# Optimization experiments

Measured on AMD Instinct MI355X. Metric: run time of the kernel, lower is better.

## Reference

```python
import jax, jax.numpy as jnp
import numpy as np

K = 64  # num_struct_elements


def rational_hat(pts, mask, centers, radius):
    """pts: (B,P,D), mask: (B,P), centers: (K,D), radius: scalar -> (B,K).

    f(x,c) = 1/(1+||x-c||_1) - 1/(1+| |r| - ||x-c||_1 |), masked sum over points.
    """
    # L1 distance to every center: (B,P,K)
    d = jnp.sum(jnp.abs(pts[:, :, None, :] - centers[None, None, :, :]), axis=-1)
    f = 1.0 / (1.0 + d) - 1.0 / (1.0 + jnp.abs(jnp.abs(radius) - d))
    # mask dummy points and reduce over the point axis -> (B,K)
    return jnp.einsum('bpk,bp->bk', f, mask)


def setup_inputs() -> dict:
    key = jax.random.key(0)
    ks = jax.random.split(key, 6)
    B, P0, PE = 128, 4096, 1024
    inp = {
        'h_0': jax.random.normal(ks[0], (B, P0, 2), dtype=jnp.float32),
        'mask_0': jnp.ones((B, P0), dtype=jnp.float32),
        'h_0_ess': jax.random.normal(ks[1], (B, PE, 1), dtype=jnp.float32),
        'mask_0_ess': jnp.ones((B, PE), dtype=jnp.float32),
        'h_1_ess': jax.random.normal(ks[2], (B, PE, 1), dtype=jnp.float32),
        'mask_1_ess': jnp.ones((B, PE), dtype=jnp.float32),
        # learned parameters: centers ~ N(0,1) (torchph default init), radius init 0.1
        'centers_0': jax.random.normal(ks[3], (K, 2), dtype=jnp.float32),
        'radius_0': jnp.float32(0.1),
        'centers_0_ess': jax.random.normal(ks[4], (K, 1), dtype=jnp.float32),
        'radius_0_ess': jnp.float32(0.1),
        'centers_1_ess': jax.random.normal(ks[5], (K, 1), dtype=jnp.float32),
        'radius_1_ess': jnp.float32(0.1),
    }
    return inp


def reference(h_0, mask_0, h_0_ess, mask_0_ess, h_1_ess, mask_1_ess,
              centers_0, radius_0, centers_0_ess, radius_0_ess,
              centers_1_ess, radius_1_ess):
    x0 = rational_hat(h_0, mask_0, centers_0, radius_0)
    x0e = rational_hat(h_0_ess, mask_0_ess, centers_0_ess, radius_0_ess)
    x1e = rational_hat(h_1_ess, mask_1_ess, centers_1_ess, radius_1_ess)
    return jnp.concatenate([x0, x0e, x1e], axis=1)  # (B, 3K)
```

## Files before the change

kernel.cpp:

```cpp
#include <hip/hip_runtime.h>

#define TPB 256
#define NW  (TPB / 64)
#define PPB 1024
#define PPW (PPB / NW)
#define PAIRS_PER_WAVE (PPW / 2)

typedef float v2f __attribute__((ext_vector_type(2)));

static __device__ __forceinline__ v2f vabs2(v2f v) {
    return __builtin_elementwise_max(v, -v);
}

__global__ __launch_bounds__(TPB) void pershom_kernel(
    const float* __restrict__ h0,  const float* __restrict__ m0,
    const float* __restrict__ h0e, const float* __restrict__ m0e,
    const float* __restrict__ h1e, const float* __restrict__ m1e,
    const float* __restrict__ c0,  const float* __restrict__ r0,
    const float* __restrict__ c0e, const float* __restrict__ r0e,
    const float* __restrict__ c1e, const float* __restrict__ r1e,
    float* __restrict__ out)
{
    __shared__ float4 pxy[PPB / 2];
    __shared__ v2f    pm [PPB / 2];
    __shared__ float  partial[NW][64];

    const int bid = blockIdx.x;
    const int tid = threadIdx.x;
    const int k   = tid & 63;
    const int sub = tid >> 6;

    const float* h; const float* m; const float* cen; const float* rad;
    int outidx, D;
    if (bid < 512) {
        int b = bid >> 2, p0 = (bid & 3) * PPB;
        h = h0 + (size_t)(b * 4096 + p0) * 2; m = m0 + b * 4096 + p0;
        cen = c0; rad = r0; outidx = b * 192 + k; D = 2;
    } else if (bid < 640) {
        int b = bid - 512;
        h = h0e + b * 1024; m = m0e + b * 1024;
        cen = c0e; rad = r0e; outidx = b * 192 + 64 + k; D = 1;
    } else {
        int b = bid - 640;
        h = h1e + b * 1024; m = m1e + b * 1024;
        cen = c1e; rad = r1e; outidx = b * 192 + 128 + k; D = 1;
    }

    if (D == 2) {
        const float4* src = (const float4*)h;
        const v2f*    msk = (const v2f*)m;
        for (int j = tid; j < PPB / 2; j += TPB) {
            float4 q = src[j];
            pxy[j] = make_float4(q.x, q.z, q.y, q.w);
            pm[j]  = msk[j];
        }
    } else {
        const v2f* src = (const v2f*)h;
        const v2f* msk = (const v2f*)m;
        for (int j = tid; j < PPB / 2; j += TPB) {
            v2f x = src[j];
            pxy[j] = make_float4(x.x, x.y, 0.f, 0.f);
            pm[j]  = msk[j];
        }
    }

    float cx, cy;
    if (D == 2) { cx = cen[2 * k]; cy = cen[2 * k + 1]; }
    else        { cx = cen[k];     cy = 0.f; }
    const float R = fabsf(rad[0]);

    __syncthreads();

    const v2f cx2 = {cx, cx}, cy2 = {cy, cy};
    const v2f one2 = {1.f, 1.f}, R2v = {R, R};
    v2f acc0 = {0.f, 0.f}, acc1 = {0.f, 0.f};
    const int base = sub * PAIRS_PER_WAVE;

    if (D == 2) {
        #pragma unroll 4
        for (int j = 0; j < PAIRS_PER_WAVE; ++j) {
            float4 q = pxy[base + j];
            v2f mm = pm[base + j];
            v2f x01 = {q.x, q.y};
            v2f y01 = {q.z, q.w};
            v2f d   = vabs2(x01 - cx2) + vabs2(y01 - cy2);
            v2f at  = vabs2(R2v - d);
            v2f num = at - d;
            v2f den = (one2 + d) * (one2 + at);
            v2f rc; rc.x = __builtin_amdgcn_rcpf(den.x);
                    rc.y = __builtin_amdgcn_rcpf(den.y);
            v2f c = (mm * num) * rc;
            if (j & 1) acc1 += c; else acc0 += c;
        }
    } else {
        #pragma unroll 4
        for (int j = 0; j < PAIRS_PER_WAVE; ++j) {
            float4 q = pxy[base + j];
            v2f mm = pm[base + j];
            v2f x01 = {q.x, q.y};
            v2f d   = vabs2(x01 - cx2);
            v2f at  = vabs2(R2v - d);
            v2f num = at - d;
            v2f den = (one2 + d) * (one2 + at);
            v2f rc; rc.x = __builtin_amdgcn_rcpf(den.x);
                    rc.y = __builtin_amdgcn_rcpf(den.y);
            v2f c = (mm * num) * rc;
            if (j & 1) acc1 += c; else acc0 += c;
        }
    }

    v2f accv = acc0 + acc1;
    partial[sub][k] = accv.x + accv.y;
    __syncthreads();
    if (tid < 64) {
        float s = 0.f;
        #pragma unroll
        for (int w = 0; w < NW; ++w) s += partial[w][tid];
        atomicAdd(&out[outidx], s);
    }
}

extern "C" void kernel_launch(void* const* d_in, const int* in_sizes, int n_in,
                              void* d_out, int out_size, void* d_ws, size_t ws_size,
                              hipStream_t stream) {
    const float* h0  = (const float*)d_in[0];
    const float* m0  = (const float*)d_in[1];
    const float* h0e = (const float*)d_in[2];
    const float* m0e = (const float*)d_in[3];
    const float* h1e = (const float*)d_in[4];
    const float* m1e = (const float*)d_in[5];
    const float* c0  = (const float*)d_in[6];
    const float* r0  = (const float*)d_in[7];
    const float* c0e = (const float*)d_in[8];
    const float* r0e = (const float*)d_in[9];
    const float* c1e = (const float*)d_in[10];
    const float* r1e = (const float*)d_in[11];
    float* out = (float*)d_out;

    hipMemsetAsync(out, 0, (size_t)out_size * sizeof(float), stream);

    dim3 grid(512 + 128 + 128);
    dim3 block(TPB);
    pershom_kernel<<<grid, block, 0, stream>>>(
        h0, m0, h0e, m0e, h1e, m1e, c0, r0, c0e, r0e, c1e, r1e, out);
}
```

Baseline: 93.45 us.

## Split D=2 work by center groups per block, drop atomics and memset

Each D=2 block now handles one batch row across all 4096 points but only 16 of the 64 centers. That lets every block write its outputs directly instead of using atomicAdd, so the memset launch is removed. Shared memory is padded (129 stride) so the 16 segments per wave avoid bank conflicts. The reciprocal is shared between two points (one rcp of the product and two multiplies), which halves the transcendental count at some precision risk from overflow or underflow of the product. Each D=2 block now loads the full 4096-point row, so global reads of h0 are repeated four times, and LDS use grows considerably.

New measurement: 95.80 us. 1.03x slower.

```diff
diff --git a/kernel.cpp b/kernel.cpp
--- a/kernel.cpp
+++ b/kernel.cpp
@@ -1,10 +1,6 @@
 #include <hip/hip_runtime.h>
 
 #define TPB 256
-#define NW  (TPB / 64)
-#define PPB 1024
-#define PPW (PPB / NW)
-#define PAIRS_PER_WAVE (PPW / 2)
 
 typedef float v2f __attribute__((ext_vector_type(2)));
 
@@ -21,102 +17,112 @@
     const float* __restrict__ c1e, const float* __restrict__ r1e,
     float* __restrict__ out)
 {
-    __shared__ float4 pxy[PPB / 2];
-    __shared__ v2f    pm [PPB / 2];
-    __shared__ float  partial[NW][64];
+    __shared__ float4 pxy[16 * 129];
+    __shared__ v2f    pm [16 * 129];
+    __shared__ float  partial[256];
 
     const int bid = blockIdx.x;
     const int tid = threadIdx.x;
-    const int k   = tid & 63;
-    const int sub = tid >> 6;
+    const v2f one2 = {1.f, 1.f};
 
-    const float* h; const float* m; const float* cen; const float* rad;
-    int outidx, D;
     if (bid < 512) {
-        int b = bid >> 2, p0 = (bid & 3) * PPB;
-        h = h0 + (size_t)(b * 4096 + p0) * 2; m = m0 + b * 4096 + p0;
-        cen = c0; rad = r0; outidx = b * 192 + k; D = 2;
-    } else if (bid < 640) {
-        int b = bid - 512;
-        h = h0e + b * 1024; m = m0e + b * 1024;
-        cen = c0e; rad = r0e; outidx = b * 192 + 64 + k; D = 1;
-    } else {
-        int b = bid - 640;
-        h = h1e + b * 1024; m = m1e + b * 1024;
-        cen = c1e; rad = r1e; outidx = b * 192 + 128 + k; D = 1;
-    }
+        const int b     = bid >> 2;
+        const int kbase = (bid & 3) * 16;
+        const float4* src = (const float4*)(h0 + (size_t)b * 4096 * 2);
+        const v2f*    msk = (const v2f*)(m0 + b * 4096);
 
-    if (D == 2) {
-        const float4* src = (const float4*)h;
-        const v2f*    msk = (const v2f*)m;
-        for (int j = tid; j < PPB / 2; j += TPB) {
-            float4 q = src[j];
-            pxy[j] = make_float4(q.x, q.z, q.y, q.w);
-            pm[j]  = msk[j];
+        for (int p = tid; p < 2048; p += TPB) {
+            float4 q = src[p];
+            int off  = (p >> 7) * 129 + (p & 127);
+            pxy[off] = make_float4(q.x, q.z, q.y, q.w);
+            pm [off] = msk[p];
         }
-    } else {
-        const v2f* src = (const v2f*)h;
-        const v2f* msk = (const v2f*)m;
-        for (int j = tid; j < PPB / 2; j += TPB) {
-            v2f x = src[j];
-            pxy[j] = make_float4(x.x, x.y, 0.f, 0.f);
-            pm[j]  = msk[j];
-        }
-    }
 
-    float cx, cy;
-    if (D == 2) { cx = cen[2 * k]; cy = cen[2 * k + 1]; }
-    else        { cx = cen[k];     cy = 0.f; }
-    const float R = fabsf(rad[0]);
+        const int k   = tid & 15;
+        const int seg = tid >> 4;
+        const float cx = c0[2 * (kbase + k)];
+        const float cy = c0[2 * (kbase + k) + 1];
+        const float R  = fabsf(r0[0]);
+        const v2f cx2 = {cx, cx}, cy2 = {cy, cy}, R2v = {R, R};
 
-    __syncthreads();
+        __syncthreads();
 
-    const v2f cx2 = {cx, cx}, cy2 = {cy, cy};
-    const v2f one2 = {1.f, 1.f}, R2v = {R, R};
-    v2f acc0 = {0.f, 0.f}, acc1 = {0.f, 0.f};
-    const int base = sub * PAIRS_PER_WAVE;
-
-    if (D == 2) {
+        v2f acc = {0.f, 0.f};
+        const int base = seg * 129;
         #pragma unroll 4
-        for (int j = 0; j < PAIRS_PER_WAVE; ++j) {
+        for (int j = 0; j < 128; ++j) {
             float4 q = pxy[base + j];
-            v2f mm = pm[base + j];
+            v2f mm   = pm [base + j];
             v2f x01 = {q.x, q.y};
             v2f y01 = {q.z, q.w};
             v2f d   = vabs2(x01 - cx2) + vabs2(y01 - cy2);
             v2f at  = vabs2(R2v - d);
             v2f num = at - d;
             v2f den = (one2 + d) * (one2 + at);
-            v2f rc; rc.x = __builtin_amdgcn_rcpf(den.x);
-                    rc.y = __builtin_amdgcn_rcpf(den.y);
-            v2f c = (mm * num) * rc;
-            if (j & 1) acc1 += c; else acc0 += c;
+            float rp = __builtin_amdgcn_rcpf(den.x * den.y);
+            v2f rc  = {den.y * rp, den.x * rp};
+            acc += (mm * num) * rc;
+        }
+
+        partial[tid] = acc.x + acc.y;
+        __syncthreads();
+        if (tid < 16) {
+            float s = 0.f;
+            #pragma unroll
+            for (int w = 0; w < 16; ++w) s += partial[w * 16 + tid];
+            out[b * 192 + kbase + tid] = s;
         }
     } else {
+        const float* h; const float* m; const float* cen; const float* rad;
+        int outoff;
+        if (bid < 640) {
+            int b = bid - 512;
+            h = h0e + b * 1024; m = m0e + b * 1024;
+            cen = c0e; rad = r0e; outoff = b * 192 + 64;
+        } else {
+            int b = bid - 640;
+            h = h1e + b * 1024; m = m1e + b * 1024;
+            cen = c1e; rad = r1e; outoff = b * 192 + 128;
+        }
+        const v2f* src = (const v2f*)h;
+        const v2f* msk = (const v2f*)m;
+        for (int j = tid; j < 512; j += TPB) {
+            v2f x = src[j];
+            pxy[j] = make_float4(x.x, x.y, 0.f, 0.f);
+            pm [j] = msk[j];
+        }
+
+        const int k   = tid & 63;
+        const int sub = tid >> 6;
+        const float cx = cen[k];
+        const float R  = fabsf(rad[0]);
+        const v2f cx2 = {cx, cx}, R2v = {R, R};
+
+        __syncthreads();
+
+        v2f acc = {0.f, 0.f};
+        const int base = sub * 128;
         #pragma unroll 4
-        for (int j = 0; j < PAIRS_PER_WAVE; ++j) {
+        for (int j = 0; j < 128; ++j) {
             float4 q = pxy[base + j];
-            v2f mm = pm[base + j];
+            v2f mm   = pm [base + j];
             v2f x01 = {q.x, q.y};
             v2f d   = vabs2(x01 - cx2);
             v2f at  = vabs2(R2v - d);
             v2f num = at - d;
             v2f den = (one2 + d) * (one2 + at);
-            v2f rc; rc.x = __builtin_amdgcn_rcpf(den.x);
-                    rc.y = __builtin_amdgcn_rcpf(den.y);
-            v2f c = (mm * num) * rc;
-            if (j & 1) acc1 += c; else acc0 += c;
+            float rp = __builtin_amdgcn_rcpf(den.x * den.y);
+            v2f rc  = {den.y * rp, den.x * rp};
+            acc += (mm * num) * rc;
         }
-    }
 
-    v2f accv = acc0 + acc1;
-    partial[sub][k] = accv.x + accv.y;
-    __syncthreads();
-    if (tid < 64) {
-        float s = 0.f;
-        #pragma unroll
-        for (int w = 0; w < NW; ++w) s += partial[w][tid];
-        atomicAdd(&out[outidx], s);
+        partial[sub * 64 + k] = acc.x + acc.y;
+        __syncthreads();
+        if (tid < 64) {
+            float s = partial[tid] + partial[64 + tid]
+                    + partial[128 + tid] + partial[192 + tid];
+            out[outoff + tid] = s;
+        }
     }
 }
 
@@ -137,8 +143,6 @@
     const float* r1e = (const float*)d_in[11];
     float* out = (float*)d_out;
 
-    hipMemsetAsync(out, 0, (size_t)out_size * sizeof(float), stream);
-
     dim3 grid(512 + 128 + 128);
     dim3 block(TPB);
     pershom_kernel<<<grid, block, 0, stream>>>(
```
